# Performance work log

Hardware: AMD Instinct MI355X
Metric: run time of the kernel (lower is better)

Reference implementation:

```python
import jax, jax.numpy as jnp
import numpy as np

H, D = 8, 16
NA, NB, E, F = 50000, 50000, 200000, 128
SQRT_D = float(np.sqrt(D))


def _proj(x, W, b):
    # Linear then split heads: [N, F] -> [N, H, D]
    return (x @ W + b).reshape(x.shape[0], H, D)


def _seg_softmax(alpha, idx, n):
    # softmax over edges sharing the same destination node (per head)
    amax = jax.ops.segment_max(alpha, idx, num_segments=n)
    amax = jnp.where(jnp.isfinite(amax), amax, 0.0)
    ex = jnp.exp(alpha - amax[idx])
    den = jax.ops.segment_sum(ex, idx, num_segments=n)
    return ex / (den[idx] + 1e-16)


def _hgt_conv(xa, xb, eis, Wk, bk, Wq, bq, Wv, bv, Wa, ba, skip, arel, mrel, prel):
    # node types: 0='a', 1='b'; edge types: 0 a->b, 1 b->a, 2 a->a
    xs = (xa, xb)
    k = [_proj(xs[t], Wk[t], bk[t]) for t in range(2)]
    q = [_proj(xs[t], Wq[t], bq[t]) for t in range(2)]
    v = [_proj(xs[t], Wv[t], bv[t]) for t in range(2)]
    nn_ = (xa.shape[0], xb.shape[0])
    agg = [jnp.zeros((nn_[t], H, D), xa.dtype) for t in range(2)]
    spec = ((0, 1, eis[0]), (1, 0, eis[1]), (0, 0, eis[2]))
    for e, (s, d, ei) in enumerate(spec):
        src, dst = ei[0], ei[1]
        k_rel = jnp.einsum('nhd,hde->nhe', k[s], arel[e])  # [Ns,H,D]
        v_rel = jnp.einsum('nhd,hde->nhe', v[s], mrel[e])
        alpha = jnp.sum(q[d][dst] * k_rel[src], axis=-1) * prel[e] / SQRT_D  # [E,H]
        w = _seg_softmax(alpha, dst, nn_[d])
        agg[d] = agg[d] + jax.ops.segment_sum(v_rel[src] * w[..., None], dst, num_segments=nn_[d])
    outs = []
    for t in range(2):
        o = jax.nn.gelu(agg[t].reshape(-1, H * D), approximate=False) @ Wa[t] + ba[t]
        sgate = jax.nn.sigmoid(skip[t])  # learned skip-gate, dims match so always applied
        outs.append(sgate * o + (1.0 - sgate) * xs[t])
    return outs[0], outs[1]


def _forward(xa, xb, eis, Wk, bk, Wq, bq, Wv, bv, Wa, ba, skip, arel, mrel, prel):
    for l in range(2):
        xa, xb = _hgt_conv(xa, xb, eis, Wk[l], bk[l], Wq[l], bq[l], Wv[l], bv[l],
                           Wa[l], ba[l], skip[l], arel[l], mrel[l], prel[l])
        if l < 1:
            xa, xb = jax.nn.relu(xa), jax.nn.relu(xb)  # dropout: identity in eval mode
    return xa, xb


def setup_inputs() -> dict:
    key = jax.random.key(0)
    ks = jax.random.split(key, 12)
    s = 0.05
    return {
        'xa': jax.random.normal(ks[0], (NA, F), jnp.float32),
        'xb': jax.random.normal(ks[1], (NB, F), jnp.float32),
        'ei_ab': jax.random.randint(ks[2], (2, E), 0, NA, dtype=jnp.int32),
        'ei_ba': jax.random.randint(ks[3], (2, E), 0, NB, dtype=jnp.int32),
        'ei_aa': jax.random.randint(ks[4], (2, E), 0, NA, dtype=jnp.int32),
        'Wk': jax.random.normal(ks[5], (2, 2, F, F), jnp.float32) * s,
        'bk': jnp.zeros((2, 2, F), jnp.float32),
        'Wq': jax.random.normal(ks[6], (2, 2, F, F), jnp.float32) * s,
        'bq': jnp.zeros((2, 2, F), jnp.float32),
        'Wv': jax.random.normal(ks[7], (2, 2, F, F), jnp.float32) * s,
        'bv': jnp.zeros((2, 2, F), jnp.float32),
        'Wa': jax.random.normal(ks[8], (2, 2, F, F), jnp.float32) * s,
        'ba': jnp.zeros((2, 2, F), jnp.float32),
        'skip': jnp.zeros((2, 2), jnp.float32),
        'arel': jax.random.normal(ks[9], (2, 3, H, D, D), jnp.float32) * (1.0 / SQRT_D),
        'mrel': jax.random.normal(ks[10], (2, 3, H, D, D), jnp.float32) * (1.0 / SQRT_D),
        'prel': jnp.ones((2, 3, H), jnp.float32),
    }


def reference(xa, xb, ei_ab, ei_ba, ei_aa, Wk, bk, Wq, bq, Wv, bv, Wa, ba, skip, arel, mrel, prel):
    return _forward(xa, xb, (ei_ab, ei_ba, ei_aa), Wk, bk, Wq, bq, Wv, bv, Wa, ba, skip, arel, mrel, prel)
```

## Files before the change

kernel.cpp:

```cpp
#include <hip/hip_runtime.h>
#include <hip/hip_bf16.h>
#include <math.h>

#define F 128
#define NH 8
#define HD 16

static inline int cdiv(int a, int b) { return (a + b - 1) / b; }

typedef __attribute__((ext_vector_type(8))) short bf16x8;
typedef __attribute__((ext_vector_type(4))) float f32x4;

__device__ __forceinline__ float geluf(float x) {
    return 0.5f * x * (1.f + erff(x * 0.70710678118654752440f));
}

__device__ __forceinline__ short f2bf(float f) {
    __hip_bfloat16 h = __float2bfloat16(f);
    return *reinterpret_cast<short*>(&h);
}

__device__ __forceinline__ float bflo(unsigned int u) { return __uint_as_float(u << 16); }
__device__ __forceinline__ float bfhi(unsigned int u) { return __uint_as_float(u & 0xffff0000u); }
__device__ __forceinline__ float bf2f(short s) {
    return __uint_as_float(((unsigned int)(unsigned short)s) << 16);
}

__device__ __forceinline__ void slot_info(int slot, int& kind, int& wsel, int& e, int& t) {
    switch (slot) {
        case 0: kind = 0; wsel = 0; t = 0; e = 0; break;
        case 1: kind = 1; wsel = 1; t = 0; e = 0; break;
        case 2: kind = 1; wsel = 2; t = 0; e = 0; break;
        case 3: kind = 1; wsel = 1; t = 0; e = 2; break;
        case 4: kind = 1; wsel = 2; t = 0; e = 2; break;
        case 5: kind = 0; wsel = 0; t = 1; e = 0; break;
        case 6: kind = 1; wsel = 1; t = 1; e = 1; break;
        case 7: kind = 1; wsel = 2; t = 1; e = 1; break;
        case 8: kind = 0; wsel = 3; t = 0; e = 0; break;
        default: kind = 0; wsel = 3; t = 1; e = 0; break;
    }
}

__global__ void prep_weights(const float* __restrict__ Wk, const float* __restrict__ bk,
                             const float* __restrict__ Wq, const float* __restrict__ bq,
                             const float* __restrict__ Wv, const float* __restrict__ bv,
                             const float* __restrict__ Wa, const float* __restrict__ ba,
                             const float* __restrict__ arel, const float* __restrict__ mrel,
                             short* __restrict__ Wslots, float* __restrict__ bslots) {
    const int WTOT = 10 * 16384;
    const int layer = blockIdx.y;
    short* Wl = Wslots + (size_t)layer * WTOT;
    float* bl = bslots + (size_t)layer * 10 * 128;
    int idx = blockIdx.x * blockDim.x + threadIdx.x;
    if (idx < WTOT) {
        int slot = idx >> 14, rem = idx & 16383;
        int n = rem >> 7, k = rem & 127;
        int kind, wsel, e, t;
        slot_info(slot, kind, wsel, e, t);
        float out;
        if (kind == 0) {
            const float* Wb = (wsel == 0 ? Wq : Wa) + (size_t)(layer * 2 + t) * 16384;
            out = Wb[k * 128 + n];
        } else {
            int h = n >> 4, j = n & 15;
            const float* Wb = (wsel == 1 ? Wk : Wv) + (size_t)(layer * 2 + t) * 16384;
            const float* R = (wsel == 1 ? arel : mrel) + (size_t)((layer * 3 + e) * NH + h) * 256;
            float s = 0.f;
            #pragma unroll
            for (int d = 0; d < HD; ++d) s += Wb[k * 128 + h * 16 + d] * R[d * 16 + j];
            out = s;
        }
        Wl[(size_t)slot * 16384 + n * 128 + k] = f2bf(out);
    } else {
        int r = idx - WTOT;
        if (r < 10 * 128) {
            int slot = r >> 7, n = r & 127;
            int kind, wsel, e, t;
            slot_info(slot, kind, wsel, e, t);
            float out;
            if (kind == 0) {
                const float* bb = (wsel == 0 ? bq : ba) + (size_t)(layer * 2 + t) * 128;
                out = bb[n];
            } else {
                int h = n >> 4, j = n & 15;
                const float* bb = (wsel == 1 ? bk : bv) + (size_t)(layer * 2 + t) * 128;
                const float* R = (wsel == 1 ? arel : mrel) + (size_t)((layer * 3 + e) * NH + h) * 256;
                float s = 0.f;
                #pragma unroll
                for (int d = 0; d < HD; ++d) s += bb[h * 16 + d] * R[d * 16 + j];
                out = s;
            }
            bl[slot * 128 + n] = out;
        }
    }
}

__device__ __forceinline__ short* qkv_slot_ptr(int side, int s,
    short* qA, short* kA0, short* vA0, short* kA2, short* vA2,
    short* qB, short* kB1, short* vB1) {
    if (side) {
        if (s == 0) return qB;
        if (s == 1) return kB1;
        return vB1;
    }
    if (s == 0) return qA;
    if (s == 1) return kA0;
    if (s == 2) return vA0;
    if (s == 3) return kA2;
    return vA2;
}

__global__ __launch_bounds__(256) void gemm_qkv_all(
    const float* __restrict__ Aa, const float* __restrict__ Ab,
    const short* __restrict__ Wl, const float* __restrict__ bl,
    short* __restrict__ qA, short* __restrict__ kA0, short* __restrict__ vA0,
    short* __restrict__ kA2, short* __restrict__ vA2,
    short* __restrict__ qB, short* __restrict__ kB1, short* __restrict__ vB1,
    int NA_, int NB_, int nbA) {
    __shared__ short Ws[128 * 136];
    __shared__ short As[64 * 136];
    float* Wsf = (float*)Ws;
    const int tid = threadIdx.x;
    const int bid = blockIdx.x;
    const int side = bid >= nbA;
    const float* A = side ? Ab : Aa;
    const int N = side ? NB_ : NA_;
    const int row0 = (side ? bid - nbA : bid) * 64;
    const short* Wbase = Wl + (side ? (size_t)5 * 16384 : 0);
    const float* bbase = bl + (side ? 5 * 128 : 0);
    const int S = side ? 3 : 5;

    #pragma unroll
    for (int it = 0; it < 4; ++it) {
        int chunk = tid + it * 256;
        int r = chunk >> 4, c8 = (chunk & 15) * 8;
        int gr = row0 + r;
        bf16x8 s = {};
        if (gr < N) {
            float4 v0 = *(const float4*)&A[(size_t)gr * F + c8];
            float4 v1 = *(const float4*)&A[(size_t)gr * F + c8 + 4];
            s[0] = f2bf(v0.x); s[1] = f2bf(v0.y); s[2] = f2bf(v0.z); s[3] = f2bf(v0.w);
            s[4] = f2bf(v1.x); s[5] = f2bf(v1.y); s[6] = f2bf(v1.z); s[7] = f2bf(v1.w);
        }
        *(bf16x8*)&As[r * 136 + c8] = s;
    }
    __syncthreads();

    const int wave = tid >> 6;
    const int lane = tid & 63;
    const int m16 = lane & 15;
    const int kg = lane >> 4;
    const int arow = wave * 16 + m16;

    bf16x8 af[4];
    #pragma unroll
    for (int kq = 0; kq < 4; ++kq)
        af[kq] = *(const bf16x8*)&As[arow * 136 + kq * 32 + kg * 8];

    for (int s = 0; s < S; ++s) {
        if (s) __syncthreads();
        const short* Wt = Wbase + (size_t)s * 16384;
        #pragma unroll
        for (int it = 0; it < 8; ++it) {
            int chunk = tid + it * 256;
            int r = chunk >> 4, c8 = (chunk & 15) * 8;
            *(int4*)&Ws[r * 136 + c8] = *(const int4*)&Wt[r * 128 + c8];
        }
        __syncthreads();

        f32x4 acc[8] = {};
        #pragma unroll
        for (int kq = 0; kq < 4; ++kq) {
            #pragma unroll
            for (int nt = 0; nt < 8; ++nt) {
                bf16x8 b = *(const bf16x8*)&Ws[(nt * 16 + m16) * 136 + kq * 32 + kg * 8];
                acc[nt] = __builtin_amdgcn_mfma_f32_16x16x32_bf16(af[kq], b, acc[nt], 0, 0, 0);
            }
        }
        __syncthreads();

        #pragma unroll
        for (int nt = 0; nt < 8; ++nt)
            #pragma unroll
            for (int r = 0; r < 4; ++r)
                Wsf[(wave * 16 + kg * 4 + r) * 132 + nt * 16 + m16] = acc[nt][r];
        __syncthreads();

        short* optr = qkv_slot_ptr(side, s, qA, kA0, vA0, kA2, vA2, qB, kB1, vB1);
        const float* bias = bbase + s * 128;
        #pragma unroll
        for (int it = 0; it < 4; ++it) {
            int chunk = tid + it * 256;
            int r = chunk >> 4, c8 = (chunk & 15) * 8;
            int gr = row0 + r;
            if (gr >= N) continue;
            float4 b0 = *(const float4*)&bias[c8];
            float4 b1 = *(const float4*)&bias[c8 + 4];
            bf16x8 o;
            o[0] = f2bf(Wsf[r * 132 + c8 + 0] + b0.x);
            o[1] = f2bf(Wsf[r * 132 + c8 + 1] + b0.y);
            o[2] = f2bf(Wsf[r * 132 + c8 + 2] + b0.z);
            o[3] = f2bf(Wsf[r * 132 + c8 + 3] + b0.w);
            o[4] = f2bf(Wsf[r * 132 + c8 + 4] + b1.x);
            o[5] = f2bf(Wsf[r * 132 + c8 + 5] + b1.y);
            o[6] = f2bf(Wsf[r * 132 + c8 + 6] + b1.z);
            o[7] = f2bf(Wsf[r * 132 + c8 + 7] + b1.w);
            *(bf16x8*)&optr[(size_t)gr * F + c8] = o;
        }
    }
}

__global__ __launch_bounds__(256) void fused_out_qkv(
    const short* __restrict__ aggA, const short* __restrict__ aggB,
    const short* __restrict__ Wl0, const float* __restrict__ bl0,
    const float* __restrict__ xfA, const float* __restrict__ xfB,
    const float* __restrict__ skipp,
    const short* __restrict__ Wl1, const float* __restrict__ bl1,
    short* __restrict__ x1A, short* __restrict__ x1B,
    short* __restrict__ qA, short* __restrict__ kA0, short* __restrict__ vA0,
    short* __restrict__ kA2, short* __restrict__ vA2,
    short* __restrict__ qB, short* __restrict__ kB1, short* __restrict__ vB1,
    int NA_, int NB_, int nbA) {
    __shared__ short Ws[128 * 136];
    __shared__ short As[64 * 136];
    float* Wsf = (float*)Ws;
    const int tid = threadIdx.x;
    const int bid = blockIdx.x;
    const int side = bid >= nbA;
    const short* A = side ? aggB : aggA;
    const int N = side ? NB_ : NA_;
    const int row0 = (side ? bid - nbA : bid) * 64;
    const short* Wt0 = Wl0 + (size_t)(side ? 9 : 8) * 16384;
    const float* bias0 = bl0 + (side ? 9 : 8) * 128;

    #pragma unroll
    for (int it = 0; it < 8; ++it) {
        int chunk = tid + it * 256;
        int r = chunk >> 4, c8 = (chunk & 15) * 8;
        *(int4*)&Ws[r * 136 + c8] = *(const int4*)&Wt0[r * 128 + c8];
    }
    #pragma unroll
    for (int it = 0; it < 4; ++it) {
        int chunk = tid + it * 256;
        int r = chunk >> 4, c8 = (chunk & 15) * 8;
        int gr = row0 + r;
        bf16x8 s = {};
        if (gr < N) {
            s = *(const bf16x8*)&A[(size_t)gr * F + c8];
            #pragma unroll
            for (int u = 0; u < 8; ++u) s[u] = f2bf(geluf(bf2f(s[u])));
        }
        *(bf16x8*)&As[r * 136 + c8] = s;
    }
    __syncthreads();

    const int wave = tid >> 6;
    const int lane = tid & 63;
    const int m16 = lane & 15;
    const int kg = lane >> 6 == 0 ? (lane >> 4) : (lane >> 4);
    const int kgv = lane >> 4;
    const int arow = wave * 16 + m16;

    {
        f32x4 acc[8] = {};
        #pragma unroll
        for (int k0 = 0; k0 < 128; k0 += 32) {
            bf16x8 a = *(const bf16x8*)&As[arow * 136 + k0 + kgv * 8];
            #pragma unroll
            for (int nt = 0; nt < 8; ++nt) {
                bf16x8 b = *(const bf16x8*)&Ws[(nt * 16 + m16) * 136 + k0 + kgv * 8];
                acc[nt] = __builtin_amdgcn_mfma_f32_16x16x32_bf16(a, b, acc[nt], 0, 0, 0);
            }
        }
        __syncthreads();
        #pragma unroll
        for (int nt = 0; nt < 8; ++nt)
            #pragma unroll
            for (int r = 0; r < 4; ++r)
                Wsf[(wave * 16 + kgv * 4 + r) * 132 + nt * 16 + m16] = acc[nt][r];
        __syncthreads();
    }

    {
        float sg = 1.f / (1.f + expf(-skipp[side]));
        short* x1 = side ? x1B : x1A;
        const float* xf = side ? xfB : xfA;
        #pragma unroll
        for (int it = 0; it < 4; ++it) {
            int chunk = tid + it * 256;
            int r = chunk >> 4, c8 = (chunk & 15) * 8;
            int gr = row0 + r;
            if (gr >= N) continue;
            float4 b0 = *(const float4*)&bias0[c8];
            float4 b1 = *(const float4*)&bias0[c8 + 4];
            float4 x0v = *(const float4*)&xf[(size_t)gr * F + c8];
            float4 x1v = *(const float4*)&xf[(size_t)gr * F + c8 + 4];
            float v[8];
            #pragma unroll
            for (int u = 0; u < 8; ++u) v[u] = Wsf[r * 132 + c8 + u];
            v[0] += b0.x; v[1] += b0.y; v[2] += b0.z; v[3] += b0.w;
            v[4] += b1.x; v[5] += b1.y; v[6] += b1.z; v[7] += b1.w;
            float xr[8] = {x0v.x, x0v.y, x0v.z, x0v.w, x1v.x, x1v.y, x1v.z, x1v.w};
            bf16x8 o;
            #pragma unroll
            for (int u = 0; u < 8; ++u)
                o[u] = f2bf(fmaxf(sg * v[u] + (1.f - sg) * xr[u], 0.f));
            *(bf16x8*)&x1[(size_t)gr * F + c8] = o;
            *(bf16x8*)&As[r * 136 + c8] = o;
        }
    }
    __syncthreads();

    bf16x8 af[4];
    #pragma unroll
    for (int kq = 0; kq < 4; ++kq)
        af[kq] = *(const bf16x8*)&As[arow * 136 + kq * 32 + kgv * 8];

    const short* Wbase = Wl1 + (side ? (size_t)5 * 16384 : 0);
    const float* bbase = bl1 + (side ? 5 * 128 : 0);
    const int S = side ? 3 : 5;

    for (int s = 0; s < S; ++s) {
        __syncthreads();
        const short* Wt = Wbase + (size_t)s * 16384;
        #pragma unroll
        for (int it = 0; it < 8; ++it) {
            int chunk = tid + it * 256;
            int r = chunk >> 4, c8 = (chunk & 15) * 8;
            *(int4*)&Ws[r * 136 + c8] = *(const int4*)&Wt[r * 128 + c8];
        }
        __syncthreads();

        f32x4 acc[8] = {};
        #pragma unroll
        for (int kq = 0; kq < 4; ++kq) {
            #pragma unroll
            for (int nt = 0; nt < 8; ++nt) {
                bf16x8 b = *(const bf16x8*)&Ws[(nt * 16 + m16) * 136 + kq * 32 + kgv * 8];
                acc[nt] = __builtin_amdgcn_mfma_f32_16x16x32_bf16(af[kq], b, acc[nt], 0, 0, 0);
            }
        }
        __syncthreads();

        #pragma unroll
        for (int nt = 0; nt < 8; ++nt)
            #pragma unroll
            for (int r = 0; r < 4; ++r)
                Wsf[(wave * 16 + kgv * 4 + r) * 132 + nt * 16 + m16] = acc[nt][r];
        __syncthreads();

        short* optr = qkv_slot_ptr(side, s, qA, kA0, vA0, kA2, vA2, qB, kB1, vB1);
        const float* bias = bbase + s * 128;
        #pragma unroll
        for (int it = 0; it < 4; ++it) {
            int chunk = tid + it * 256;
            int r = chunk >> 4, c8 = (chunk & 15) * 8;
            int gr = row0 + r;
            if (gr >= N) continue;
            float4 b0 = *(const float4*)&bias[c8];
            float4 b1 = *(const float4*)&bias[c8 + 4];
            bf16x8 o;
            o[0] = f2bf(Wsf[r * 132 + c8 + 0] + b0.x);
            o[1] = f2bf(Wsf[r * 132 + c8 + 1] + b0.y);
            o[2] = f2bf(Wsf[r * 132 + c8 + 2] + b0.z);
            o[3] = f2bf(Wsf[r * 132 + c8 + 3] + b0.w);
            o[4] = f2bf(Wsf[r * 132 + c8 + 4] + b1.x);
            o[5] = f2bf(Wsf[r * 132 + c8 + 5] + b1.y);
            o[6] = f2bf(Wsf[r * 132 + c8 + 6] + b1.z);
            o[7] = f2bf(Wsf[r * 132 + c8 + 7] + b1.w);
            *(bf16x8*)&optr[(size_t)gr * F + c8] = o;
        }
    }
}

__global__ __launch_bounds__(256) void gemm_out_final(
    const short* __restrict__ aggA, const short* __restrict__ aggB,
    const short* __restrict__ Wl, const float* __restrict__ bl,
    const short* __restrict__ xbA, const short* __restrict__ xbB,
    const float* __restrict__ skipp,
    float* __restrict__ CfA, float* __restrict__ CfB,
    int NA_, int NB_, int nbA) {
    __shared__ short Ws[128 * 136];
    __shared__ short As[64 * 136];
    float* Wsf = (float*)Ws;
    const int tid = threadIdx.x;
    const int bid = blockIdx.x;
    const int side = bid >= nbA;
    const short* A = side ? aggB : aggA;
    const int N = side ? NB_ : NA_;
    const int row0 = (side ? bid - nbA : bid) * 64;
    const short* Wt = Wl + (size_t)(side ? 9 : 8) * 16384;
    const float* bias = bl + (side ? 9 : 8) * 128;

    #pragma unroll
    for (int it = 0; it < 8; ++it) {
        int chunk = tid + it * 256;
        int r = chunk >> 4, c8 = (chunk & 15) * 8;
        *(int4*)&Ws[r * 136 + c8] = *(const int4*)&Wt[r * 128 + c8];
    }
    #pragma unroll
    for (int it = 0; it < 4; ++it) {
        int chunk = tid + it * 256;
        int r = chunk >> 4, c8 = (chunk & 15) * 8;
        int gr = row0 + r;
        bf16x8 s = {};
        if (gr < N) {
            s = *(const bf16x8*)&A[(size_t)gr * F + c8];
            #pragma unroll
            for (int u = 0; u < 8; ++u) s[u] = f2bf(geluf(bf2f(s[u])));
        }
        *(bf16x8*)&As[r * 136 + c8] = s;
    }
    __syncthreads();

    const int wave = tid >> 6;
    const int lane = tid & 63;
    const int m16 = lane & 15;
    const int kg = lane >> 4;
    const int arow = wave * 16 + m16;

    f32x4 acc[8] = {};
    #pragma unroll
    for (int k0 = 0; k0 < 128; k0 += 32) {
        bf16x8 a = *(const bf16x8*)&As[arow * 136 + k0 + kg * 8];
        #pragma unroll
        for (int nt = 0; nt < 8; ++nt) {
            bf16x8 b = *(const bf16x8*)&Ws[(nt * 16 + m16) * 136 + k0 + kg * 8];
            acc[nt] = __builtin_amdgcn_mfma_f32_16x16x32_bf16(a, b, acc[nt], 0, 0, 0);
        }
    }
    __syncthreads();

    #pragma unroll
    for (int nt = 0; nt < 8; ++nt)
        #pragma unroll
        for (int r = 0; r < 4; ++r)
            Wsf[(wave * 16 + kg * 4 + r) * 132 + nt * 16 + m16] = acc[nt][r];
    __syncthreads();

    float sg = 1.f / (1.f + expf(-skipp[side]));
    #pragma unroll
    for (int it = 0; it < 4; ++it) {
        int chunk = tid + it * 256;
        int r = chunk >> 4, c8 = (chunk & 15) * 8;
        int gr = row0 + r;
        if (gr >= N) continue;
        float4 b0 = *(const float4*)&bias[c8];
        float4 b1 = *(const float4*)&bias[c8 + 4];
        float v[8];
        #pragma unroll
        for (int u = 0; u < 8; ++u) v[u] = Wsf[r * 132 + c8 + u];
        v[0] += b0.x; v[1] += b0.y; v[2] += b0.z; v[3] += b0.w;
        v[4] += b1.x; v[5] += b1.y; v[6] += b1.z; v[7] += b1.w;
        const short* xb = side ? xbB : xbA;
        bf16x8 xrv = *(const bf16x8*)&xb[(size_t)gr * F + c8];
        float* Cf = side ? CfB : CfA;
        float o[8];
        #pragma unroll
        for (int u = 0; u < 8; ++u)
            o[u] = sg * v[u] + (1.f - sg) * bf2f(xrv[u]);
        *(float4*)&Cf[(size_t)gr * F + c8]     = make_float4(o[0], o[1], o[2], o[3]);
        *(float4*)&Cf[(size_t)gr * F + c8 + 4] = make_float4(o[4], o[5], o[6], o[7]);
    }
}


__global__ void hist_all(const int* __restrict__ ei0, const int* __restrict__ ei1,
                         const int* __restrict__ ei2, int E0, int E1, int E2,
                         int NB_, int NA_, int* __restrict__ cnt) {
    int i = blockIdx.x * 256 + threadIdx.x;
    if (i >= E0 + E1 + E2) return;
    const int* ei; int li, Ee, base;
    if (i < E0)           { li = i;           ei = ei0; Ee = E0; base = 0; }
    else if (i < E0 + E1) { li = i - E0;      ei = ei1; Ee = E1; base = NB_; }
    else                  { li = i - E0 - E1; ei = ei2; Ee = E2; base = NB_ + NA_; }
    atomicAdd(&cnt[base + ei[Ee + li]], 1);
}

__global__ void scan1(const int* __restrict__ cnt, int n, int* __restrict__ off,
                      int* __restrict__ bsum) {
    __shared__ int lds[256];
    int tid = threadIdx.x, i = blockIdx.x * 256 + tid;
    int v = (i < n) ? cnt[i] : 0;
    lds[tid] = v;
    __syncthreads();
    #pragma unroll
    for (int s = 1; s < 256; s <<= 1) {
        int t = (tid >= s) ? lds[tid - s] : 0;
        __syncthreads();
        lds[tid] += t;
        __syncthreads();
    }
    if (i < n) off[i] = lds[tid] - v;
    if (tid == 255) bsum[blockIdx.x] = lds[255];
}

__global__ __launch_bounds__(1024) void scan2(int* __restrict__ bsum, int nb,
                                              int* __restrict__ off_n) {
    __shared__ int lds[1024];
    int tid = threadIdx.x;
    int v = (tid < nb) ? bsum[tid] : 0;
    lds[tid] = v;
    __syncthreads();
    #pragma unroll
    for (int s = 1; s < 1024; s <<= 1) {
        int t = (tid >= s) ? lds[tid - s] : 0;
        __syncthreads();
        lds[tid] += t;
        __syncthreads();
    }
    if (tid < nb) bsum[tid] = lds[tid] - v;
    if (tid == 1023) *off_n = lds[1023];
}

__global__ void scan3(int* __restrict__ off, int* __restrict__ woff,
                      const int* __restrict__ bsum, int n) {
    int i = blockIdx.x * 256 + threadIdx.x;
    if (i < n) {
        int v = off[i] + bsum[blockIdx.x];
        off[i] = v;
        woff[i] = v;
    }
}

__global__ void scatter_all(const int* __restrict__ ei0, const int* __restrict__ ei1,
                            const int* __restrict__ ei2, int E0, int E1, int E2,
                            int NB_, int NA_, int* __restrict__ woff,
                            int* __restrict__ csr_src) {
    int i = blockIdx.x * 256 + threadIdx.x;
    if (i >= E0 + E1 + E2) return;
    const int* ei; int li, Ee, base;
    if (i < E0)           { li = i;           ei = ei0; Ee = E0; base = 0; }
    else if (i < E0 + E1) { li = i - E0;      ei = ei1; Ee = E1; base = NB_; }
    else                  { li = i - E0 - E1; ei = ei2; Ee = E2; base = NB_ + NA_; }
    int p = atomicAdd(&woff[base + ei[Ee + li]], 1);
    csr_src[p] = ei[li] * 64;
}

#define CH 8

__device__ __forceinline__ void seg_set(
    const unsigned int* __restrict__ kArr, const unsigned int* __restrict__ vArr,
    int c0, int e0, const int* __restrict__ csr_src, int l,
    float qlo, float qhi, float pr, float& rlo, float& rhi) {
    float den = 0.f, alo = 0.f, ahi = 0.f;
    while (c0 < e0) {
        int n = e0 - c0; if (n > CH) n = CH;
        int sj[CH];
        unsigned int ku[CH], vu[CH];
        #pragma unroll
        for (int c = 0; c < CH; ++c) if (c < n) sj[c] = csr_src[c0 + c];
        #pragma unroll
        for (int c = 0; c < CH; ++c) if (c < n) {
            ku[c] = kArr[sj[c] + l];
            vu[c] = vArr[sj[c] + l];
        }
        #pragma unroll
        for (int c = 0; c < CH; ++c) if (c < n) {
            float p = bflo(ku[c]) * qlo + bfhi(ku[c]) * qhi;
            p += __shfl_xor(p, 4, 8);
            p += __shfl_xor(p, 2, 8);
            p += __shfl_xor(p, 1, 8);
            float ex = __expf(fminf(p * pr, 80.f));
            den += ex;
            alo = fmaf(ex, bflo(vu[c]), alo);
            ahi = fmaf(ex, bfhi(vu[c]), ahi);
        }
        c0 += n;
    }
    float inv = 1.f / (den + 1e-16f);
    rlo = fmaf(alo, inv, rlo);
    rhi = fmaf(ahi, inv, rhi);
}

__global__ __launch_bounds__(256) void seg_attn_all(
    const short* __restrict__ qA, const short* __restrict__ kA0,
    const short* __restrict__ vA0, const short* __restrict__ kA2,
    const short* __restrict__ vA2, const short* __restrict__ qB,
    const short* __restrict__ kB1, const short* __restrict__ vB1,
    const int* __restrict__ off0, const int* __restrict__ off1,
    const int* __restrict__ off2, const int* __restrict__ csrS,
    const float* __restrict__ prelL,
    short* __restrict__ aggA, short* __restrict__ aggB,
    int NA_, int NB_, int nba) {
    int l = threadIdx.x & 63;
    int h = l >> 3;
    float rlo = 0.f, rhi = 0.f;
    if ((int)blockIdx.x < nba) {
        int dst = blockIdx.x * 4 + (threadIdx.x >> 6);
        if (dst >= NA_) return;
        unsigned int qu = ((const unsigned int*)qA)[(size_t)dst * 64 + l];
        float qlo = bflo(qu), qhi = bfhi(qu);
        seg_set((const unsigned int*)kB1, (const unsigned int*)vB1,
                off1[dst], off1[dst + 1], csrS, l, qlo, qhi,
                prelL[1 * NH + h] * 0.25f, rlo, rhi);
        seg_set((const unsigned int*)kA2, (const unsigned int*)vA2,
                off2[dst], off2[dst + 1], csrS, l, qlo, qhi,
                prelL[2 * NH + h] * 0.25f, rlo, rhi);
        unsigned int plo = (unsigned int)(unsigned short)f2bf(rlo);
        unsigned int phi = (unsigned int)(unsigned short)f2bf(rhi);
        ((unsigned int*)aggA)[(size_t)dst * 64 + l] = plo | (phi << 16);
    } else {
        int dst = (blockIdx.x - nba) * 4 + (threadIdx.x >> 6);
        if (dst >= NB_) return;
        unsigned int qu = ((const unsigned int*)qB)[(size_t)dst * 64 + l];
        float qlo = bflo(qu), qhi = bfhi(qu);
        seg_set((const unsigned int*)kA0, (const unsigned int*)vA0,
                off0[dst], off0[dst + 1], csrS, l, qlo, qhi,
                prelL[0 * NH + h] * 0.25f, rlo, rhi);
        unsigned int plo = (unsigned int)(unsigned short)f2bf(rlo);
        unsigned int phi = (unsigned int)(unsigned short)f2bf(rhi);
        ((unsigned int*)aggB)[(size_t)dst * 64 + l] = plo | (phi << 16);
    }
}

extern "C" void kernel_launch(void* const* d_in, const int* in_sizes, int n_in,
                              void* d_out, int out_size, void* d_ws, size_t ws_size,
                              hipStream_t stream) {
    const float* xa   = (const float*)d_in[0];
    const float* xb   = (const float*)d_in[1];
    const int* ei_ab  = (const int*)d_in[2];
    const int* ei_ba  = (const int*)d_in[3];
    const int* ei_aa  = (const int*)d_in[4];
    const float* Wk   = (const float*)d_in[5];
    const float* bk   = (const float*)d_in[6];
    const float* Wq   = (const float*)d_in[7];
    const float* bq   = (const float*)d_in[8];
    const float* Wv   = (const float*)d_in[9];
    const float* bv   = (const float*)d_in[10];
    const float* Wa   = (const float*)d_in[11];
    const float* ba   = (const float*)d_in[12];
    const float* skip = (const float*)d_in[13];
    const float* arel = (const float*)d_in[14];
    const float* mrel = (const float*)d_in[15];
    const float* prel = (const float*)d_in[16];

    const int NA = in_sizes[0] / F;
    const int NB = in_sizes[1] / F;
    const int E0 = in_sizes[2] / 2, E1 = in_sizes[3] / 2, E2 = in_sizes[4] / 2;
    const int ET = E0 + E1 + E2;
    const int NT = NB + NA + NA;

    float* ws = (float*)d_ws;
    size_t o = 0;
    float* bslots = ws + o; o += 2 * 10 * 128;
    int* iws = (int*)(ws + o);
    size_t io = 0;
    int* cnt   = iws + io; io += NT;
    int* bsum  = iws + io; io += 1024;
    int* offc  = iws + io; io += NT + 1;
    int* woff  = iws + io; io += NT;
    int* csrS  = iws + io; io += ET;
    io = (io + 7) & ~(size_t)7;
    short* sws = (short*)(iws + io);
    size_t so = 0;
    short* qA  = sws + so; so += (size_t)NA * 128;
    short* kA0 = sws + so; so += (size_t)NA * 128;
    short* vA0 = sws + so; so += (size_t)NA * 128;
    short* kA2 = sws + so; so += (size_t)NA * 128;
    short* vA2 = sws + so; so += (size_t)NA * 128;
    short* qB  = sws + so; so += (size_t)NB * 128;
    short* kB1 = sws + so; so += (size_t)NB * 128;
    short* vB1 = sws + so; so += (size_t)NB * 128;
    short* aggA = sws + so; so += (size_t)NA * 128;
    short* aggB = sws + so; so += (size_t)NB * 128;
    short* x1ab = sws + so; so += (size_t)NA * 128;
    short* x1bb = sws + so; so += (size_t)NB * 128;
    short* Wslots = sws + so; so += (size_t)2 * 10 * 16384;

    float* outA = (float*)d_out;
    float* outB = (float*)d_out + (size_t)NA * F;

    {
        dim3 g(cdiv(10 * 16384 + 10 * 128, 256), 2);
        prep_weights<<<g, 256, 0, stream>>>(Wk, bk, Wq, bq, Wv, bv, Wa, ba,
                                            arel, mrel, Wslots, bslots);
    }

    hipMemsetAsync(cnt, 0, (size_t)NT * sizeof(int), stream);
    hist_all<<<cdiv(ET, 256), 256, 0, stream>>>(ei_ab, ei_ba, ei_aa, E0, E1, E2, NB, NA, cnt);
    {
        int nb = cdiv(NT, 256);
        scan1<<<nb, 256, 0, stream>>>(cnt, NT, offc, bsum);
        scan2<<<1, 1024, 0, stream>>>(bsum, nb, offc + NT);
        scan3<<<nb, 256, 0, stream>>>(offc, woff, bsum, NT);
    }
    scatter_all<<<cdiv(ET, 256), 256, 0, stream>>>(ei_ab, ei_ba, ei_aa, E0, E1, E2, NB, NA, woff, csrS);

    const int* off_e0 = offc;
    const int* off_e1 = offc + NB;
    const int* off_e2 = offc + NB + NA;

    const int nbA64 = cdiv(NA, 64), nbB64 = cdiv(NB, 64);
    const int nba4 = cdiv(NA, 4), nbb4 = cdiv(NB, 4);

    const short* Wl0 = Wslots;
    const short* Wl1 = Wslots + (size_t)10 * 16384;
    const float* bl0 = bslots;
    const float* bl1 = bslots + 10 * 128;

    gemm_qkv_all<<<nbA64 + nbB64, 256, 0, stream>>>(
        xa, xb, Wl0, bl0, qA, kA0, vA0, kA2, vA2, qB, kB1, vB1, NA, NB, nbA64);

    seg_attn_all<<<nba4 + nbb4, 256, 0, stream>>>(
        qA, kA0, vA0, kA2, vA2, qB, kB1, vB1,
        off_e0, off_e1, off_e2, csrS, prel, aggA, aggB, NA, NB, nba4);

    fused_out_qkv<<<nbA64 + nbB64, 256, 0, stream>>>(
        aggA, aggB, Wl0, bl0, xa, xb, skip, Wl1, bl1,
        x1ab, x1bb, qA, kA0, vA0, kA2, vA2, qB, kB1, vB1, NA, NB, nbA64);

    seg_attn_all<<<nba4 + nbb4, 256, 0, stream>>>(
        qA, kA0, vA0, kA2, vA2, qB, kB1, vB1,
        off_e0, off_e1, off_e2, csrS, prel + 3 * NH, aggA, aggB, NA, NB, nba4);

    gemm_out_final<<<nbA64 + nbB64, 256, 0, stream>>>(
        aggA, aggB, Wl1, bl1, x1ab, x1bb, skip + 2, outA, outB, NA, NB, nbA64);
}
```

Baseline: 360.2 us.

## Process four edges per wave with 16-byte loads in segment attention

Restructures the per-destination attention kernel so each wave splits into four 16-lane groups. Each group handles a different edge, and each lane loads 8 bf16 values (uint4) instead of 2. Partial sums and denominators are combined across groups with shuffles at the end, and CSR indices are rescaled to uint4 units. The aim is more memory-level parallelism and wider gathers on the edge loop. The cost is extra fold shuffles, idle groups when a segment's degree is not a multiple of four, and higher register use.

```diff
diff --git a/kernel.cpp b/kernel.cpp
--- a/kernel.cpp
+++ b/kernel.cpp
@@ -24,6 +24,9 @@
 __device__ __forceinline__ float bfhi(unsigned int u) { return __uint_as_float(u & 0xffff0000u); }
 __device__ __forceinline__ float bf2f(short s) {
     return __uint_as_float(((unsigned int)(unsigned short)s) << 16);
+}
+__device__ __forceinline__ unsigned int packbf(float a, float b) {
+    return (unsigned int)(unsigned short)f2bf(a) | ((unsigned int)(unsigned short)f2bf(b) << 16);
 }
 
 __device__ __forceinline__ void slot_info(int slot, int& kind, int& wsel, int& e, int& t) {
@@ -257,7 +260,6 @@
     const int wave = tid >> 6;
     const int lane = tid & 63;
     const int m16 = lane & 15;
-    const int kg = lane >> 6 == 0 ? (lane >> 4) : (lane >> 4);
     const int kgv = lane >> 4;
     const int arow = wave * 16 + m16;
 
@@ -534,43 +536,55 @@
     else if (i < E0 + E1) { li = i - E0;      ei = ei1; Ee = E1; base = NB_; }
     else                  { li = i - E0 - E1; ei = ei2; Ee = E2; base = NB_ + NA_; }
     int p = atomicAdd(&woff[base + ei[Ee + li]], 1);
-    csr_src[p] = ei[li] * 64;
-}
-
-#define CH 8
-
-__device__ __forceinline__ void seg_set(
-    const unsigned int* __restrict__ kArr, const unsigned int* __restrict__ vArr,
-    int c0, int e0, const int* __restrict__ csr_src, int l,
-    float qlo, float qhi, float pr, float& rlo, float& rhi) {
-    float den = 0.f, alo = 0.f, ahi = 0.f;
-    while (c0 < e0) {
-        int n = e0 - c0; if (n > CH) n = CH;
-        int sj[CH];
-        unsigned int ku[CH], vu[CH];
-        #pragma unroll
-        for (int c = 0; c < CH; ++c) if (c < n) sj[c] = csr_src[c0 + c];
-        #pragma unroll
-        for (int c = 0; c < CH; ++c) if (c < n) {
-            ku[c] = kArr[sj[c] + l];
-            vu[c] = vArr[sj[c] + l];
-        }
-        #pragma unroll
-        for (int c = 0; c < CH; ++c) if (c < n) {
-            float p = bflo(ku[c]) * qlo + bfhi(ku[c]) * qhi;
-            p += __shfl_xor(p, 4, 8);
-            p += __shfl_xor(p, 2, 8);
-            p += __shfl_xor(p, 1, 8);
-            float ex = __expf(fminf(p * pr, 80.f));
-            den += ex;
-            alo = fmaf(ex, bflo(vu[c]), alo);
-            ahi = fmaf(ex, bfhi(vu[c]), ahi);
-        }
-        c0 += n;
-    }
+    csr_src[p] = ei[li] * 16;
+}
+
+__device__ __forceinline__ void seg_set4(
+    const uint4* __restrict__ kArr, const uint4* __restrict__ vArr,
+    int c0, int e1, const int* __restrict__ csr, int s, int p,
+    const float* __restrict__ qf, float pr,
+    float* __restrict__ accv, float& den) {
+    for (; c0 < e1; c0 += 4) {
+        int rem = e1 - c0;
+        bool act = s < rem;
+        int sj = csr[c0 + (act ? s : 0)];
+        uint4 kw = kArr[sj + p];
+        uint4 vw = vArr[sj + p];
+        float d = bflo(kw.x) * qf[0];
+        d = fmaf(bfhi(kw.x), qf[1], d);
+        d = fmaf(bflo(kw.y), qf[2], d);
+        d = fmaf(bfhi(kw.y), qf[3], d);
+        d = fmaf(bflo(kw.z), qf[4], d);
+        d = fmaf(bfhi(kw.z), qf[5], d);
+        d = fmaf(bflo(kw.w), qf[6], d);
+        d = fmaf(bfhi(kw.w), qf[7], d);
+        d += __shfl_xor(d, 1);
+        float ex = __expf(fminf(d * pr, 80.f));
+        ex = act ? ex : 0.f;
+        den += ex;
+        accv[0] = fmaf(ex, bflo(vw.x), accv[0]);
+        accv[1] = fmaf(ex, bfhi(vw.x), accv[1]);
+        accv[2] = fmaf(ex, bflo(vw.y), accv[2]);
+        accv[3] = fmaf(ex, bfhi(vw.y), accv[3]);
+        accv[4] = fmaf(ex, bflo(vw.z), accv[4]);
+        accv[5] = fmaf(ex, bfhi(vw.z), accv[5]);
+        accv[6] = fmaf(ex, bflo(vw.w), accv[6]);
+        accv[7] = fmaf(ex, bfhi(vw.w), accv[7]);
+    }
+}
+
+__device__ __forceinline__ void seg_fold(float* __restrict__ accv, float& den,
+                                         float* __restrict__ r) {
+    #pragma unroll
+    for (int j = 0; j < 8; ++j) {
+        accv[j] += __shfl_xor(accv[j], 16);
+        accv[j] += __shfl_xor(accv[j], 32);
+    }
+    den += __shfl_xor(den, 16);
+    den += __shfl_xor(den, 32);
     float inv = 1.f / (den + 1e-16f);
-    rlo = fmaf(alo, inv, rlo);
-    rhi = fmaf(ahi, inv, rhi);
+    #pragma unroll
+    for (int j = 0; j < 8; ++j) r[j] = fmaf(accv[j], inv, r[j]);
 }
 
 __global__ __launch_bounds__(256) void seg_attn_all(
@@ -583,34 +597,44 @@
     const float* __restrict__ prelL,
     short* __restrict__ aggA, short* __restrict__ aggB,
     int NA_, int NB_, int nba) {
-    int l = threadIdx.x & 63;
-    int h = l >> 3;
-    float rlo = 0.f, rhi = 0.f;
-    if ((int)blockIdx.x < nba) {
-        int dst = blockIdx.x * 4 + (threadIdx.x >> 6);
-        if (dst >= NA_) return;
-        unsigned int qu = ((const unsigned int*)qA)[(size_t)dst * 64 + l];
-        float qlo = bflo(qu), qhi = bfhi(qu);
-        seg_set((const unsigned int*)kB1, (const unsigned int*)vB1,
-                off1[dst], off1[dst + 1], csrS, l, qlo, qhi,
-                prelL[1 * NH + h] * 0.25f, rlo, rhi);
-        seg_set((const unsigned int*)kA2, (const unsigned int*)vA2,
-                off2[dst], off2[dst + 1], csrS, l, qlo, qhi,
-                prelL[2 * NH + h] * 0.25f, rlo, rhi);
-        unsigned int plo = (unsigned int)(unsigned short)f2bf(rlo);
-        unsigned int phi = (unsigned int)(unsigned short)f2bf(rhi);
-        ((unsigned int*)aggA)[(size_t)dst * 64 + l] = plo | (phi << 16);
+    const int wv = threadIdx.x >> 6;
+    const int l = threadIdx.x & 63;
+    const int s = l >> 4;
+    const int p = l & 15;
+    const int h = p >> 1;
+    const int isA = (int)blockIdx.x < nba;
+    int dst = (isA ? blockIdx.x : blockIdx.x - nba) * 4 + wv;
+    if (dst >= (isA ? NA_ : NB_)) return;
+
+    uint4 qw = ((const uint4*)(isA ? qA : qB))[(size_t)dst * 16 + p];
+    float qf[8] = {bflo(qw.x), bfhi(qw.x), bflo(qw.y), bfhi(qw.y),
+                   bflo(qw.z), bfhi(qw.z), bflo(qw.w), bfhi(qw.w)};
+
+    float r[8] = {};
+    float accv[8] = {};
+    float den = 0.f;
+    if (isA) {
+        seg_set4((const uint4*)kB1, (const uint4*)vB1, off1[dst], off1[dst + 1],
+                 csrS, s, p, qf, prelL[1 * NH + h] * 0.25f, accv, den);
+        seg_fold(accv, den, r);
+        #pragma unroll
+        for (int j = 0; j < 8; ++j) accv[j] = 0.f;
+        den = 0.f;
+        seg_set4((const uint4*)kA2, (const uint4*)vA2, off2[dst], off2[dst + 1],
+                 csrS, s, p, qf, prelL[2 * NH + h] * 0.25f, accv, den);
+        seg_fold(accv, den, r);
     } else {
-        int dst = (blockIdx.x - nba) * 4 + (threadIdx.x >> 6);
-        if (dst >= NB_) return;
-        unsigned int qu = ((const unsigned int*)qB)[(size_t)dst * 64 + l];
-        float qlo = bflo(qu), qhi = bfhi(qu);
-        seg_set((const unsigned int*)kA0, (const unsigned int*)vA0,
-                off0[dst], off0[dst + 1], csrS, l, qlo, qhi,
-                prelL[0 * NH + h] * 0.25f, rlo, rhi);
-        unsigned int plo = (unsigned int)(unsigned short)f2bf(rlo);
-        unsigned int phi = (unsigned int)(unsigned short)f2bf(rhi);
-        ((unsigned int*)aggB)[(size_t)dst * 64 + l] = plo | (phi << 16);
+        seg_set4((const uint4*)kA0, (const uint4*)vA0, off0[dst], off0[dst + 1],
+                 csrS, s, p, qf, prelL[0 * NH + h] * 0.25f, accv, den);
+        seg_fold(accv, den, r);
+    }
+    if (s == 0) {
+        uint4 o;
+        o.x = packbf(r[0], r[1]);
+        o.y = packbf(r[2], r[3]);
+        o.z = packbf(r[4], r[5]);
+        o.w = packbf(r[6], r[7]);
+        ((uint4*)(isA ? aggA : aggB))[(size_t)dst * 16 + p] = o;
     }
 }
 
```

After: 341.2 us. 1.06x faster.
